# Performance work log

Measured on AMD Instinct MI355X. Metric: run time of the kernel, lower is better.

## Reference

```python
import jax, jax.numpy as jnp
import numpy as np

B, L = 2, 1024
D_MODEL, N_LAYER = 768, 2
D_INNER, D_STATE, D_CONV, DT_RANK = 1536, 16, 4, 48
D_INT, VOCAB = 1536, 32000
EPS = 1e-5


def layernorm(x, w, b):
    m = x.mean(-1, keepdims=True)
    v = ((x - m) ** 2).mean(-1, keepdims=True)
    return (x - m) * jax.lax.rsqrt(v + EPS) * w + b


def silu(x):
    return x * jax.nn.sigmoid(x)


def depthwise_causal_conv(x, w, b):
    # x: (B,L,D); w: (D,K) torch depthwise weight squeezed; b: (D,)
    k = w.shape[-1]
    kern = w.T[:, None, :]  # (K,1,D) for 'WIO' with feature_group_count=D
    y = jax.lax.conv_general_dilated(
        x, kern, window_strides=(1,), padding=[(k - 1, 0)],
        dimension_numbers=('NWC', 'WIO', 'NWC'),
        feature_group_count=x.shape[-1])
    return y + b


def selective_scan(u, delta, A, Bm, Cm, Dp):
    # u, delta: (B,L,Dn); A: (Dn,N); Bm, Cm: (B,L,N); Dp: (Dn,)
    dA = jnp.exp(delta[..., None] * A)                         # (B,L,Dn,N)
    dBu = delta[..., None] * Bm[:, :, None, :] * u[..., None]  # (B,L,Dn,N)

    def step(h, inp):
        dA_t, dBu_t, C_t = inp
        h = dA_t * h + dBu_t
        return h, jnp.einsum('bdn,bn->bd', h, C_t)

    h0 = jnp.zeros((u.shape[0], A.shape[0], A.shape[1]), u.dtype)
    _, ys = jax.lax.scan(step, h0, (jnp.swapaxes(dA, 0, 1), jnp.swapaxes(dBu, 0, 1), jnp.swapaxes(Cm, 0, 1)))
    return jnp.swapaxes(ys, 0, 1) + u * Dp


def mamba_mixer(x, p):
    xz = x @ p['in_proj'].T                     # (B,L,2*Dn)
    xin, z = jnp.split(xz, 2, axis=-1)
    xc = silu(depthwise_causal_conv(xin, p['conv_w'], p['conv_b']))
    x_dbl = xc @ p['x_proj'].T                  # (B,L,dt_rank+2N)
    dt, Bm, Cm = jnp.split(x_dbl, [DT_RANK, DT_RANK + D_STATE], axis=-1)
    delta = jax.nn.softplus(dt @ p['dt_w'].T + p['dt_b'])
    A = -jnp.exp(p['A_log'])
    y = selective_scan(xc, delta, A, Bm, Cm, p['D'])
    y = y * silu(z)
    return y @ p['out_proj'].T


def block(h, res, p):
    # mamba_ssm Block (non-fused path) with GatedMLP
    res = h + res if res is not None else h
    x = layernorm(res, p['norm_w'], p['norm_b'])
    x = mamba_mixer(x, p)
    res = x + res
    x = layernorm(res, p['norm2_w'], p['norm2_b'])
    y, gate = jnp.split(x @ p['fc1'].T, 2, axis=-1)
    x = (y * silu(gate)) @ p['fc2'].T
    return x, res


def _forward(input_ids, embed, norm_w, norm_b, in_proj, conv_w, conv_b, x_proj,
             dt_w, dt_b, A_log, D, out_proj, norm2_w, norm2_b, fc1, fc2,
             normf_w, normf_b):
    h = embed[input_ids]
    res = None
    for i in range(N_LAYER):
        p = dict(norm_w=norm_w[i], norm_b=norm_b[i], in_proj=in_proj[i],
                 conv_w=conv_w[i], conv_b=conv_b[i], x_proj=x_proj[i],
                 dt_w=dt_w[i], dt_b=dt_b[i], A_log=A_log[i], D=D[i],
                 out_proj=out_proj[i], norm2_w=norm2_w[i], norm2_b=norm2_b[i],
                 fc1=fc1[i], fc2=fc2[i])
        h_f, r_f = block(h, res, p)
        h_f = layernorm(h_f, normf_w, normf_b)
        res_flip = res[:, ::-1] if res is not None else None
        h_b, r_b = block(h[:, ::-1], res_flip, p)
        h_b = layernorm(h_b, normf_w, normf_b)
        h = h_f + h_b[:, ::-1]
        res = r_f + r_b[:, ::-1]
    # dropout is identity at inference
    res = h + res
    h = layernorm(res, normf_w, normf_b)
    return h.mean(axis=1)  # (B, d_model)


def setup_inputs() -> dict:
    key = jax.random.key(0)
    ks = iter(jax.random.split(key, 32))

    def rn(shape, scale=0.02):
        return jax.random.normal(next(ks), shape, jnp.float32) * scale

    inp = {}
    inp['input_ids'] = jax.random.randint(next(ks), (B, L), 0, VOCAB)
    inp['embed'] = rn((VOCAB, D_MODEL))
    inp['norm_w'] = jnp.ones((N_LAYER, D_MODEL), jnp.float32)
    inp['norm_b'] = jnp.zeros((N_LAYER, D_MODEL), jnp.float32)
    inp['in_proj'] = rn((N_LAYER, 2 * D_INNER, D_MODEL))
    inp['conv_w'] = rn((N_LAYER, D_INNER, D_CONV), 0.2)
    inp['conv_b'] = jnp.zeros((N_LAYER, D_INNER), jnp.float32)
    inp['x_proj'] = rn((N_LAYER, DT_RANK + 2 * D_STATE, D_INNER))
    inp['dt_w'] = rn((N_LAYER, D_INNER, DT_RANK), 0.1)
    # inverse-softplus of ~0.01 so delta starts small (matches mamba dt init spirit)
    inp['dt_b'] = jnp.full((N_LAYER, D_INNER), float(np.log(np.expm1(0.01))), jnp.float32)
    # S4D-real init: A = -(1..d_state)
    inp['A_log'] = jnp.broadcast_to(jnp.log(jnp.arange(1, D_STATE + 1, dtype=jnp.float32)), (N_LAYER, D_INNER, D_STATE)).copy()
    inp['D'] = jnp.ones((N_LAYER, D_INNER), jnp.float32)
    inp['out_proj'] = rn((N_LAYER, D_MODEL, D_INNER))
    inp['norm2_w'] = jnp.ones((N_LAYER, D_MODEL), jnp.float32)
    inp['norm2_b'] = jnp.zeros((N_LAYER, D_MODEL), jnp.float32)
    inp['fc1'] = rn((N_LAYER, 2 * D_INT, D_MODEL))
    inp['fc2'] = rn((N_LAYER, D_MODEL, D_INT))
    inp['normf_w'] = jnp.ones((D_MODEL,), jnp.float32)
    inp['normf_b'] = jnp.zeros((D_MODEL,), jnp.float32)
    return inp


def reference(input_ids, embed, norm_w, norm_b, in_proj, conv_w, conv_b, x_proj,
              dt_w, dt_b, A_log, D, out_proj, norm2_w, norm2_b, fc1, fc2,
              normf_w, normf_b):
    return _forward(input_ids, embed, norm_w, norm_b, in_proj, conv_w, conv_b,
                    x_proj, dt_w, dt_b, A_log, D, out_proj, norm2_w, norm2_b,
                    fc1, fc2, normf_w, normf_b)
```

## Files before the change

kernel.cpp:

```cpp
#include <hip/hip_runtime.h>
#include <cstddef>

#define BB 2
#define LL 1024
#define DM 768
#define DI 1536
#define NST 16
#define DTR 48
#define DINT 1536
#define NLAYER 2
#define ML (BB*LL)
#define NCH 32
#define CLEN (LL/NCH)

typedef __attribute__((ext_vector_type(8))) short s16x8;
typedef __attribute__((ext_vector_type(4))) float f32x4;

static __device__ __forceinline__ float sigm(float x){ return 1.f/(1.f+__expf(-x)); }
static __device__ __forceinline__ float silu_(float x){ return x*sigm(x); }
static __device__ __forceinline__ float softplus_(float x){ return fmaxf(x,0.f)+log1pf(__expf(-fabsf(x))); }
static __device__ __forceinline__ unsigned short f2b(float x){
  unsigned int u = __float_as_uint(x);
  unsigned int r = (u + 0x7fffu + ((u>>16)&1u)) >> 16;
  return (unsigned short)r;
}
static __device__ __forceinline__ float b2f(unsigned short v){
  return __uint_as_float(((unsigned int)v) << 16);
}

__global__ void k_embed(const int* __restrict__ ids, const float* __restrict__ emb,
                        float* __restrict__ out){
  int idx = blockIdx.x*256 + threadIdx.x;
  if (idx >= ML*DM) return;
  int c = idx % DM; int bl = idx / DM;
  out[idx] = emb[(size_t)ids[bl]*DM + c];
}

__global__ void k_add(const float* __restrict__ a, const float* __restrict__ b,
                      float* __restrict__ c, int n){
  int idx = blockIdx.x*256 + threadIdx.x;
  if (idx >= n) return;
  c[idx] = a[idx] + b[idx];
}

__global__ void k_f2b(const float* __restrict__ in, unsigned short* __restrict__ out, int n){
  int idx = blockIdx.x*256 + threadIdx.x;
  if (idx >= n) return;
  out[idx] = f2b(in[idx]);
}

__global__ void k_weff(const float* __restrict__ dw, const float* __restrict__ xp,
                       unsigned short* __restrict__ wbig){
  int idx = blockIdx.x*256 + threadIdx.x;
  int j = idx % DI, i = idx / DI;
  float s = 0.f;
  #pragma unroll
  for (int k = 0; k < DTR; k++) s += dw[i*DTR + k] * xp[(size_t)k*DI + j];
  wbig[idx] = f2b(s);
}

__global__ void k_wtail(const float* __restrict__ xp, unsigned short* __restrict__ wbig){
  int idx = blockIdx.x*256 + threadIdx.x;
  if (idx >= 128*DI) return;
  int j = idx % DI, r = idx / DI;
  unsigned short v = (r < 32) ? f2b(xp[(size_t)(DTR + r)*DI + j]) : (unsigned short)0;
  wbig[(size_t)(DI + r)*DI + j] = v;
}

__global__ __launch_bounds__(256) void k_ln(const float* __restrict__ x,
    const float* __restrict__ add, const float* __restrict__ w, const float* __restrict__ bi,
    float* __restrict__ sumout, float* __restrict__ fout, unsigned short* __restrict__ bout,
    int acc, int rows){
  int wv = threadIdx.x >> 6, lane = threadIdx.x & 63;
  int row = blockIdx.x*4 + wv;
  if (row >= rows) return;
  const float* xr = x + (size_t)row*DM;
  float v[12]; float s = 0.f, sq = 0.f;
  #pragma unroll
  for (int i = 0; i < 12; i++){
    int c = lane + 64*i;
    float t = xr[c];
    if (add) t += add[(size_t)row*DM + c];
    if (sumout) sumout[(size_t)row*DM + c] = t;
    v[i] = t; s += t; sq += t*t;
  }
  #pragma unroll
  for (int o = 32; o; o >>= 1){ s += __shfl_xor(s, o, 64); sq += __shfl_xor(sq, o, 64); }
  float mean = s*(1.f/DM);
  float var  = sq*(1.f/DM) - mean*mean;
  float rstd = rsqrtf(var + 1e-5f);
  #pragma unroll
  for (int i = 0; i < 12; i++){
    int c = lane + 64*i;
    float o = (v[i]-mean)*rstd*w[c] + bi[c];
    if (fout){
      float oo = o;
      if (acc) oo += fout[(size_t)row*DM + c];
      fout[(size_t)row*DM + c] = oo;
    }
    if (bout) bout[(size_t)row*DM + c] = f2b(o);
  }
}

static __device__ __forceinline__ void mgemm_core(
    const unsigned short* __restrict__ A, const unsigned short* __restrict__ W, int K,
    unsigned short* As, unsigned short* Bs, f32x4 (&acc)[4][4]){
  int t = threadIdx.x;
  int m0 = blockIdx.y*128, n0 = blockIdx.x*128;
  int lane = t & 63, w = t >> 6;
  int wm = w & 1, wn = w >> 1;
  for (int k0 = 0; k0 < K; k0 += 32){
    #pragma unroll
    for (int si = 0; si < 2; si++){
      int s = t + si*256;
      int row = ((s>>6)<<4) + (s & 15);
      int ko  = ((s>>4) & 3) << 3;
      *(uint4*)&As[s*8] = *(const uint4*)&A[(size_t)(m0+row)*K + k0 + ko];
      *(uint4*)&Bs[s*8] = *(const uint4*)&W[(size_t)(n0+row)*K + k0 + ko];
    }
    __syncthreads();
    s16x8 af[4], bf[4];
    #pragma unroll
    for (int i = 0; i < 4; i++) af[i] = *(const s16x8*)&As[((wm*4+i)*64 + lane)*8];
    #pragma unroll
    for (int j = 0; j < 4; j++) bf[j] = *(const s16x8*)&Bs[((wn*4+j)*64 + lane)*8];
    #pragma unroll
    for (int i = 0; i < 4; i++)
      #pragma unroll
      for (int j = 0; j < 4; j++)
        acc[i][j] = __builtin_amdgcn_mfma_f32_16x16x32_bf16(af[i], bf[j], acc[i][j], 0, 0, 0);
    __syncthreads();
  }
}

__global__ __launch_bounds__(256) void k_mgemm0(const unsigned short* __restrict__ A,
    const unsigned short* __restrict__ W, const float* __restrict__ addsrc,
    float* __restrict__ Cf, int N, int K){
  __shared__ __align__(16) unsigned short As[4096], Bs[4096];
  f32x4 acc[4][4] = {};
  mgemm_core(A, W, K, As, Bs, acc);
  int t = threadIdx.x, lane = t & 63, w = t >> 6;
  int wm = w & 1, wn = w >> 1;
  int m0 = blockIdx.y*128, n0 = blockIdx.x*128;
  int cl = lane & 15, qd = lane >> 4;
  #pragma unroll
  for (int i = 0; i < 4; i++){
    int mbase = m0 + (wm*4+i)*16 + qd*4;
    #pragma unroll
    for (int j = 0; j < 4; j++){
      int n = n0 + (wn*4+j)*16 + cl;
      #pragma unroll
      for (int r = 0; r < 4; r++){
        int m = mbase + r;
        float v = acc[i][j][r];
        if (addsrc) v += addsrc[(size_t)(m & (ML-1))*N + n];
        Cf[(size_t)m*N + n] = v;
      }
    }
  }
}

__global__ __launch_bounds__(256) void k_mgemm1(const unsigned short* __restrict__ A,
    const unsigned short* __restrict__ W, const float* __restrict__ dtb,
    unsigned short* __restrict__ dlb, float* __restrict__ bcout, int K){
  __shared__ __align__(16) unsigned short As[4096], Bs[4096];
  f32x4 acc[4][4] = {};
  mgemm_core(A, W, K, As, Bs, acc);
  int t = threadIdx.x, lane = t & 63, w = t >> 6;
  int wm = w & 1, wn = w >> 1;
  int m0 = blockIdx.y*128, n0 = blockIdx.x*128;
  int cl = lane & 15, qd = lane >> 4;
  #pragma unroll
  for (int i = 0; i < 4; i++){
    int mbase = m0 + (wm*4+i)*16 + qd*4;
    #pragma unroll
    for (int j = 0; j < 4; j++){
      int n = n0 + (wn*4+j)*16 + cl;
      #pragma unroll
      for (int r = 0; r < 4; r++){
        int m = mbase + r;
        float v = acc[i][j][r];
        if (n < DI) dlb[(size_t)m*DI + n] = f2b(softplus_(v + dtb[n]));
        else if (n < DI + 32) bcout[(size_t)m*32 + (n - DI)] = v;
      }
    }
  }
}

__global__ __launch_bounds__(256) void k_mgemm2(const unsigned short* __restrict__ A,
    const unsigned short* __restrict__ W, unsigned short* __restrict__ Cb, int N, int K){
  __shared__ __align__(16) unsigned short As[4096], Bs[4096];
  f32x4 acc[4][4] = {};
  mgemm_core(A, W, K, As, Bs, acc);
  int t = threadIdx.x, lane = t & 63, w = t >> 6;
  int wm = w & 1, wn = w >> 1;
  int m0 = blockIdx.y*128, n0 = blockIdx.x*128;
  int cl = lane & 15, qd = lane >> 4;
  #pragma unroll
  for (int i = 0; i < 4; i++){
    int mbase = m0 + (wm*4+i)*16 + qd*4;
    #pragma unroll
    for (int j = 0; j < 4; j++){
      int n = n0 + (wn*4+j)*16 + cl;
      #pragma unroll
      for (int r = 0; r < 4; r++){
        int m = mbase + r;
        Cb[(size_t)m*N + n] = f2b(acc[i][j][r]);
      }
    }
  }
}

__global__ void k_conv(const float* __restrict__ xz, const float* __restrict__ w,
                       const float* __restrict__ bi, unsigned short* __restrict__ xcb){
  int idx = blockIdx.x*256 + threadIdx.x;
  if (idx >= 2*ML*DI) return;
  int d = idx % DI; int r = idx / DI;
  int bl = r % ML; int dir = r / ML;
  int t = bl % LL; int b = bl / LL;
  float acc = bi[d];
  #pragma unroll
  for (int k = 0; k < 4; k++){
    int tp = dir ? (t + 3 - k) : (t - 3 + k);
    if (tp >= 0 && tp < LL)
      acc += w[d*4 + k] * xz[((size_t)(b*LL + tp))*(2*DI) + d];
  }
  xcb[idx] = f2b(silu_(acc));
}

__global__ __launch_bounds__(256) void k_scan1(
    const unsigned short* __restrict__ dlb, const unsigned short* __restrict__ xcb,
    const float* __restrict__ bc, const float* __restrict__ A_log,
    float* __restrict__ sA, float* __restrict__ sH){
  __shared__ float Bsh[CLEN*16];
  int blk = blockIdx.x;
  int dgrp = blk % (DI/256); int rest = blk / (DI/256);
  int ch = rest % NCH; rest /= NCH;
  int b = rest & 1; int dir = rest >> 1;
  int d = dgrp*256 + threadIdx.x;
  int t0 = dir ? (LL-1 - ch*CLEN) : ch*CLEN;
  long step = dir ? -1 : 1;
  long row0 = (long)dir*ML + b*LL + t0;
  #pragma unroll
  for (int rep = 0; rep < CLEN*16/256; rep++){
    int e = threadIdx.x + rep*256;
    int s = e >> 4, n = e & 15;
    Bsh[e] = bc[(size_t)(row0 + s*step)*32 + n];
  }
  __syncthreads();
  float ea[16];
  #pragma unroll
  for (int n = 0; n < 16; n++) ea[n] = -__expf(A_log[d*16 + n]) * 1.44269504f;
  float h[16], P[16];
  #pragma unroll
  for (int n = 0; n < 16; n++){ h[n] = 0.f; P[n] = 1.f; }
  long row = row0;
  for (int s = 0; s < CLEN; s++){
    float de = b2f(dlb[(size_t)row*DI + d]);
    float u  = b2f(xcb[(size_t)row*DI + d]);
    float duu = de*u;
    float Ba[16];
    const f32x4* Bv = (const f32x4*)&Bsh[s*16];
    *(f32x4*)&Ba[0] = Bv[0]; *(f32x4*)&Ba[4] = Bv[1];
    *(f32x4*)&Ba[8] = Bv[2]; *(f32x4*)&Ba[12] = Bv[3];
    #pragma unroll
    for (int n = 0; n < 16; n++){
      float dA = exp2f(de*ea[n]);
      h[n] = dA*h[n] + duu*Ba[n];
      P[n] *= dA;
    }
    row += step;
  }
  size_t sbase = ((((size_t)dir*BB + b)*NCH + ch)*DI + d)*16;
  #pragma unroll
  for (int n = 0; n < 16; n++){ sA[sbase+n] = P[n]; sH[sbase+n] = h[n]; }
}

__global__ __launch_bounds__(256) void k_prefix(
    const float* __restrict__ sA, const float* __restrict__ sH, float* __restrict__ h0){
  int gid = blockIdx.x*256 + threadIdx.x;
  int dn = gid % (DI*16);
  int db_ = gid / (DI*16);
  float h = 0.f;
  size_t base = (size_t)db_*NCH*DI*16 + dn;
  for (int ch = 0; ch < NCH; ch++){
    size_t idx = base + (size_t)ch*DI*16;
    h0[idx] = h;
    h = sH[idx] + sA[idx]*h;
  }
}

__global__ __launch_bounds__(256) void k_scan2(
    const unsigned short* __restrict__ dlb, const unsigned short* __restrict__ xcb,
    const float* __restrict__ bc, const float* __restrict__ xz,
    const float* __restrict__ A_log, const float* __restrict__ Dp,
    const float* __restrict__ h0, unsigned short* __restrict__ y){
  __shared__ float BCs[CLEN*32];
  int blk = blockIdx.x;
  int dgrp = blk % (DI/256); int rest = blk / (DI/256);
  int ch = rest % NCH; rest /= NCH;
  int b = rest & 1; int dir = rest >> 1;
  int d = dgrp*256 + threadIdx.x;
  int t0 = dir ? (LL-1 - ch*CLEN) : ch*CLEN;
  long step = dir ? -1 : 1;
  long row0 = (long)dir*ML + b*LL + t0;
  #pragma unroll
  for (int rep = 0; rep < CLEN*32/256; rep++){
    int e = threadIdx.x + rep*256;
    int s = e >> 5, n = e & 31;
    BCs[e] = bc[(size_t)(row0 + s*step)*32 + n];
  }
  __syncthreads();
  float ea[16];
  #pragma unroll
  for (int n = 0; n < 16; n++) ea[n] = -__expf(A_log[d*16 + n]) * 1.44269504f;
  float dD = Dp[d];
  float h[16];
  size_t hbase = ((((size_t)dir*BB + b)*NCH + ch)*DI + d)*16;
  #pragma unroll
  for (int n = 0; n < 16; n++) h[n] = h0[hbase + n];
  long row = row0;
  long zoff = (long)dir*ML;
  for (int s = 0; s < CLEN; s++){
    float de = b2f(dlb[(size_t)row*DI + d]);
    float u  = b2f(xcb[(size_t)row*DI + d]);
    float z  = xz[(size_t)(row - zoff)*(2*DI) + DI + d];
    float duu = de*u;
    float Ba[16], Ca[16];
    const f32x4* Bv = (const f32x4*)&BCs[s*32];
    *(f32x4*)&Ba[0] = Bv[0]; *(f32x4*)&Ba[4] = Bv[1];
    *(f32x4*)&Ba[8] = Bv[2]; *(f32x4*)&Ba[12] = Bv[3];
    *(f32x4*)&Ca[0] = Bv[4]; *(f32x4*)&Ca[4] = Bv[5];
    *(f32x4*)&Ca[8] = Bv[6]; *(f32x4*)&Ca[12] = Bv[7];
    float p0 = 0.f, p1 = 0.f, p2 = 0.f, p3 = 0.f;
    #pragma unroll
    for (int n = 0; n < 16; n += 4){
      float dA0 = exp2f(de*ea[n]),   dA1 = exp2f(de*ea[n+1]);
      float dA2 = exp2f(de*ea[n+2]), dA3 = exp2f(de*ea[n+3]);
      h[n]   = dA0*h[n]   + duu*Ba[n];
      h[n+1] = dA1*h[n+1] + duu*Ba[n+1];
      h[n+2] = dA2*h[n+2] + duu*Ba[n+2];
      h[n+3] = dA3*h[n+3] + duu*Ba[n+3];
      p0 = fmaf(h[n],   Ca[n],   p0);
      p1 = fmaf(h[n+1], Ca[n+1], p1);
      p2 = fmaf(h[n+2], Ca[n+2], p2);
      p3 = fmaf(h[n+3], Ca[n+3], p3);
    }
    float p = (p0+p1) + (p2+p3);
    y[(size_t)row*DI + d] = f2b((p + u*dD) * silu_(z));
    row += step;
  }
}

__global__ void k_gate(const unsigned short* __restrict__ fc1o, unsigned short* __restrict__ g){
  int idx = blockIdx.x*256 + threadIdx.x;
  if (idx >= 2*ML*DINT) return;
  int i = idx % DINT; int bl = idx / DINT;
  float aa = b2f(fc1o[(size_t)bl*2*DINT + i]);
  float gt = b2f(fc1o[(size_t)bl*2*DINT + DINT + i]);
  g[idx] = f2b(aa * silu_(gt));
}

__global__ void k_mean(const float* __restrict__ x, float* __restrict__ out){
  int d = blockIdx.x*256 + threadIdx.x;
  int b = blockIdx.y;
  if (d >= DM) return;
  float s = 0.f;
  for (int t = 0; t < LL; t++) s += x[((size_t)(b*LL + t))*DM + d];
  out[b*DM + d] = s*(1.f/LL);
}

extern "C" void kernel_launch(void* const* d_in, const int* in_sizes, int n_in,
                              void* d_out, int out_size, void* d_ws, size_t ws_size,
                              hipStream_t stream){
  const int*   ids     = (const int*)d_in[0];
  const float* embed   = (const float*)d_in[1];
  const float* norm_w  = (const float*)d_in[2];
  const float* norm_b  = (const float*)d_in[3];
  const float* in_proj = (const float*)d_in[4];
  const float* conv_w  = (const float*)d_in[5];
  const float* conv_b  = (const float*)d_in[6];
  const float* x_proj  = (const float*)d_in[7];
  const float* dt_w    = (const float*)d_in[8];
  const float* dt_b    = (const float*)d_in[9];
  const float* A_log   = (const float*)d_in[10];
  const float* Dp      = (const float*)d_in[11];
  const float* out_pj  = (const float*)d_in[12];
  const float* norm2_w = (const float*)d_in[13];
  const float* norm2_b = (const float*)d_in[14];
  const float* fc1     = (const float*)d_in[15];
  const float* fc2     = (const float*)d_in[16];
  const float* normf_w = (const float*)d_in[17];
  const float* normf_b = (const float*)d_in[18];
  float* out = (float*)d_out;

  const size_t BLD   = (size_t)ML*DM;
  const size_t BLDI  = (size_t)ML*DI;
  const size_t BL2DI = (size_t)ML*2*DI;
  const size_t SUMN  = (size_t)2*BB*NCH*DI*16;

  float* f = (float*)d_ws; size_t off = 0;
  float* h     = f+off; off += BLD;
  float* res   = f+off; off += BLD;
  float* rc    = f+off; off += BLD;
  float* resd  = f+off; off += 2*BLD;
  float* xz    = f+off; off += BL2DI;
  float* bc    = f+off; off += (size_t)2*ML*32;
  float* sA    = f+off; off += SUMN;
  float* sH    = f+off; off += SUMN;
  float* h0    = f+off; off += SUMN;
  float*          mlpo = xz;
  unsigned short* gb   = (unsigned short*)sA;
  unsigned short* u16 = (unsigned short*)(f + off); size_t uo = 0;
  unsigned short* xlnb = u16+uo; uo += BLD;
  unsigned short* x2b  = u16+uo; uo += 2*BLD;
  unsigned short* xcb  = u16+uo; uo += 2*BLDI;
  unsigned short* dlb  = u16+uo; uo += 2*BLDI;
  unsigned short* wib  = u16+uo; uo += (size_t)2*DI*DM;
  unsigned short* wob  = u16+uo; uo += (size_t)DM*DI;
  unsigned short* wbig = u16+uo; uo += (size_t)1664*DI;
  unsigned short* yb   = xcb;
  unsigned short* fc1o = xcb;
  unsigned short* wf1b = wib;
  unsigned short* wf2b = wob;
  (void)ws_size; (void)in_sizes; (void)n_in; (void)out_size;

  dim3 blk(256);
  auto cdiv = [](int a, int b){ return (a + b - 1)/b; };
  const int scan_blocks = 2*2*NCH*(DI/256);

  k_embed<<<cdiv(ML*DM,256), blk, 0, stream>>>(ids, embed, h);

  for (int l = 0; l < NLAYER; l++){
    const float* nw  = norm_w  + l*DM;
    const float* nb  = norm_b  + l*DM;
    const float* ip  = in_proj + (size_t)l*2*DI*DM;
    const float* cw  = conv_w  + (size_t)l*DI*4;
    const float* cb  = conv_b  + (size_t)l*DI;
    const float* xp  = x_proj  + (size_t)l*(DTR+2*NST)*DI;
    const float* dw  = dt_w    + (size_t)l*DI*DTR;
    const float* db  = dt_b    + (size_t)l*DI;
    const float* al  = A_log   + (size_t)l*DI*NST;
    const float* dpl = Dp      + (size_t)l*DI;
    const float* op  = out_pj  + (size_t)l*DM*DI;
    const float* n2w = norm2_w + l*DM;
    const float* n2b = norm2_b + l*DM;
    const float* f1  = fc1 + (size_t)l*2*DINT*DM;
    const float* f2  = fc2 + (size_t)l*DM*DINT;

    k_f2b<<<cdiv(2*DI*DM,256), blk, 0, stream>>>(ip, wib, 2*DI*DM);
    k_f2b<<<cdiv(DM*DI,256), blk, 0, stream>>>(op, wob, DM*DI);
    k_weff<<<cdiv(DI*DI,256), blk, 0, stream>>>(dw, xp, wbig);
    k_wtail<<<cdiv(128*DI,256), blk, 0, stream>>>(xp, wbig);

    k_ln<<<ML/4, blk, 0, stream>>>(h, (l==0)?nullptr:res, nw, nb, rc, nullptr, xlnb, 0, ML);
    k_mgemm0<<<dim3(2*DI/128, ML/128), blk, 0, stream>>>(xlnb, wib, nullptr, xz, 2*DI, DM);
    k_conv<<<cdiv(2*ML*DI,256), blk, 0, stream>>>(xz, cw, cb, xcb);
    k_mgemm1<<<dim3(1664/128, 2*ML/128), blk, 0, stream>>>(xcb, wbig, db, dlb, bc, DI);
    k_scan1<<<scan_blocks, blk, 0, stream>>>(dlb, xcb, bc, al, sA, sH);
    k_prefix<<<(2*BB*DI*16)/256, blk, 0, stream>>>(sA, sH, h0);
    k_scan2<<<scan_blocks, blk, 0, stream>>>(dlb, xcb, bc, xz, al, dpl, h0, yb);
    k_f2b<<<cdiv(2*DINT*DM,256), blk, 0, stream>>>(f1, wf1b, 2*DINT*DM);
    k_mgemm0<<<dim3(DM/128, 2*ML/128), blk, 0, stream>>>(yb, wob, rc, resd, DM, DI);
    k_f2b<<<cdiv(DM*DINT,256), blk, 0, stream>>>(f2, wf2b, DM*DINT);
    k_ln<<<2*ML/4, blk, 0, stream>>>(resd, nullptr, n2w, n2b, nullptr, nullptr, x2b, 0, 2*ML);
    k_mgemm2<<<dim3(2*DINT/128, 2*ML/128), blk, 0, stream>>>(x2b, wf1b, fc1o, 2*DINT, DM);
    k_gate<<<cdiv(2*ML*DINT,256), blk, 0, stream>>>(fc1o, gb);
    k_mgemm0<<<dim3(DM/128, 2*ML/128), blk, 0, stream>>>(gb, wf2b, nullptr, mlpo, DM, DINT);
    k_ln<<<ML/4, blk, 0, stream>>>(mlpo, nullptr, normf_w, normf_b, nullptr, h, nullptr, 0, ML);
    k_ln<<<ML/4, blk, 0, stream>>>(mlpo + BLD, nullptr, normf_w, normf_b, nullptr, h, nullptr, 1, ML);
    k_add<<<cdiv(ML*DM,256), blk, 0, stream>>>(resd, resd + BLD, res, ML*DM);
  }

  k_ln<<<ML/4, blk, 0, stream>>>(h, res, normf_w, normf_b, nullptr, rc, nullptr, 0, ML);
  k_mean<<<dim3(3, BB), blk, 0, stream>>>(rc, out);
}
```

Before: 1.286 ms.

## Batch weight conversion, shrink GEMM N-tile, store xz in bf16, fuse final layernorms

All bf16 weight conversions for both layers now run up front in one segmented kernel, plus a merged dt/x_proj weight builder. The GEMM tile shrinks from 128x128 to 128x64 to launch more blocks on the small-N projections. The in_proj output xz is stored as bf16 instead of fp32, which halves its traffic in conv and scan2 at some precision cost. The two per-branch layernorms and the residual add are fused into one kernel, and the prefix kernel writes h0 in place over sA to save a buffer.

```diff
diff --git a/kernel.cpp b/kernel.cpp
--- a/kernel.cpp
+++ b/kernel.cpp
@@ -36,41 +36,39 @@
   out[idx] = emb[(size_t)ids[bl]*DM + c];
 }
 
-__global__ void k_add(const float* __restrict__ a, const float* __restrict__ b,
-                      float* __restrict__ c, int n){
+struct Seg8 { const float* src[8]; unsigned short* dst[8]; int cum[9]; };
+__global__ void k_f2bseg(Seg8 p){
   int idx = blockIdx.x*256 + threadIdx.x;
-  if (idx >= n) return;
-  c[idx] = a[idx] + b[idx];
-}
-
-__global__ void k_f2b(const float* __restrict__ in, unsigned short* __restrict__ out, int n){
+  if (idx >= p.cum[8]) return;
+  int s = 0;
+  #pragma unroll
+  for (int i = 1; i < 8; i++) s += (idx >= p.cum[i]);
+  int local = idx - p.cum[s];
+  p.dst[s][local] = f2b(p.src[s][local]);
+}
+
+__global__ void k_wbig(const float* __restrict__ dw, const float* __restrict__ xp,
+                       unsigned short* __restrict__ wb){
   int idx = blockIdx.x*256 + threadIdx.x;
-  if (idx >= n) return;
-  out[idx] = f2b(in[idx]);
-}
-
-__global__ void k_weff(const float* __restrict__ dw, const float* __restrict__ xp,
-                       unsigned short* __restrict__ wbig){
-  int idx = blockIdx.x*256 + threadIdx.x;
+  if (idx >= 1664*DI) return;
   int j = idx % DI, i = idx / DI;
-  float s = 0.f;
-  #pragma unroll
-  for (int k = 0; k < DTR; k++) s += dw[i*DTR + k] * xp[(size_t)k*DI + j];
-  wbig[idx] = f2b(s);
-}
-
-__global__ void k_wtail(const float* __restrict__ xp, unsigned short* __restrict__ wbig){
-  int idx = blockIdx.x*256 + threadIdx.x;
-  if (idx >= 128*DI) return;
-  int j = idx % DI, r = idx / DI;
-  unsigned short v = (r < 32) ? f2b(xp[(size_t)(DTR + r)*DI + j]) : (unsigned short)0;
-  wbig[(size_t)(DI + r)*DI + j] = v;
+  unsigned short v;
+  if (i < DI){
+    float s = 0.f;
+    #pragma unroll
+    for (int k = 0; k < DTR; k++) s += dw[i*DTR + k] * xp[(size_t)k*DI + j];
+    v = f2b(s);
+  } else {
+    int r = i - DI;
+    v = (r < 32) ? f2b(xp[(size_t)(DTR + r)*DI + j]) : (unsigned short)0;
+  }
+  wb[idx] = v;
 }
 
 __global__ __launch_bounds__(256) void k_ln(const float* __restrict__ x,
     const float* __restrict__ add, const float* __restrict__ w, const float* __restrict__ bi,
     float* __restrict__ sumout, float* __restrict__ fout, unsigned short* __restrict__ bout,
-    int acc, int rows){
+    int rows){
   int wv = threadIdx.x >> 6, lane = threadIdx.x & 63;
   int row = blockIdx.x*4 + wv;
   if (row >= rows) return;
@@ -93,20 +91,48 @@
   for (int i = 0; i < 12; i++){
     int c = lane + 64*i;
     float o = (v[i]-mean)*rstd*w[c] + bi[c];
-    if (fout){
-      float oo = o;
-      if (acc) oo += fout[(size_t)row*DM + c];
-      fout[(size_t)row*DM + c] = oo;
-    }
+    if (fout) fout[(size_t)row*DM + c] = o;
     if (bout) bout[(size_t)row*DM + c] = f2b(o);
+  }
+}
+
+__global__ __launch_bounds__(256) void k_lnfin(const float* __restrict__ mlpo,
+    const float* __restrict__ resd, const float* __restrict__ w, const float* __restrict__ bi,
+    float* __restrict__ h, float* __restrict__ res){
+  int wv = threadIdx.x >> 6, lane = threadIdx.x & 63;
+  int row = blockIdx.x*4 + wv;
+  if (row >= ML) return;
+  const float* x0 = mlpo + (size_t)row*DM;
+  const float* x1 = mlpo + (size_t)(ML + row)*DM;
+  float v0[12], v1[12]; float s0=0,q0=0,s1=0,q1=0;
+  #pragma unroll
+  for (int i = 0; i < 12; i++){
+    int c = lane + 64*i;
+    float a = x0[c], b = x1[c];
+    v0[i]=a; v1[i]=b; s0+=a; q0+=a*a; s1+=b; q1+=b*b;
+  }
+  #pragma unroll
+  for (int o = 32; o; o >>= 1){
+    s0 += __shfl_xor(s0, o, 64); q0 += __shfl_xor(q0, o, 64);
+    s1 += __shfl_xor(s1, o, 64); q1 += __shfl_xor(q1, o, 64);
+  }
+  float m0 = s0*(1.f/DM), m1 = s1*(1.f/DM);
+  float r0 = rsqrtf(q0*(1.f/DM) - m0*m0 + 1e-5f);
+  float r1 = rsqrtf(q1*(1.f/DM) - m1*m1 + 1e-5f);
+  #pragma unroll
+  for (int i = 0; i < 12; i++){
+    int c = lane + 64*i;
+    float o = ((v0[i]-m0)*r0 + (v1[i]-m1)*r1)*w[c] + 2.f*bi[c];
+    h[(size_t)row*DM + c] = o;
+    res[(size_t)row*DM + c] = resd[(size_t)row*DM + c] + resd[(size_t)(ML+row)*DM + c];
   }
 }
 
 static __device__ __forceinline__ void mgemm_core(
     const unsigned short* __restrict__ A, const unsigned short* __restrict__ W, int K,
-    unsigned short* As, unsigned short* Bs, f32x4 (&acc)[4][4]){
+    unsigned short* As, unsigned short* Bs, f32x4 (&acc)[4][2]){
   int t = threadIdx.x;
-  int m0 = blockIdx.y*128, n0 = blockIdx.x*128;
+  int m0 = blockIdx.y*128, n0 = blockIdx.x*64;
   int lane = t & 63, w = t >> 6;
   int wm = w & 1, wn = w >> 1;
   for (int k0 = 0; k0 < K; k0 += 32){
@@ -116,39 +142,44 @@
       int row = ((s>>6)<<4) + (s & 15);
       int ko  = ((s>>4) & 3) << 3;
       *(uint4*)&As[s*8] = *(const uint4*)&A[(size_t)(m0+row)*K + k0 + ko];
+    }
+    {
+      int s = t;
+      int row = ((s>>6)<<4) + (s & 15);
+      int ko  = ((s>>4) & 3) << 3;
       *(uint4*)&Bs[s*8] = *(const uint4*)&W[(size_t)(n0+row)*K + k0 + ko];
     }
     __syncthreads();
-    s16x8 af[4], bf[4];
+    s16x8 af[4], bf[2];
     #pragma unroll
     for (int i = 0; i < 4; i++) af[i] = *(const s16x8*)&As[((wm*4+i)*64 + lane)*8];
     #pragma unroll
-    for (int j = 0; j < 4; j++) bf[j] = *(const s16x8*)&Bs[((wn*4+j)*64 + lane)*8];
+    for (int j = 0; j < 2; j++) bf[j] = *(const s16x8*)&Bs[((wn*2+j)*64 + lane)*8];
     #pragma unroll
     for (int i = 0; i < 4; i++)
       #pragma unroll
-      for (int j = 0; j < 4; j++)
+      for (int j = 0; j < 2; j++)
         acc[i][j] = __builtin_amdgcn_mfma_f32_16x16x32_bf16(af[i], bf[j], acc[i][j], 0, 0, 0);
     __syncthreads();
   }
 }
 
-__global__ __launch_bounds__(256) void k_mgemm0(const unsigned short* __restrict__ A,
+__global__ __launch_bounds__(256) void k_mg0(const unsigned short* __restrict__ A,
     const unsigned short* __restrict__ W, const float* __restrict__ addsrc,
     float* __restrict__ Cf, int N, int K){
-  __shared__ __align__(16) unsigned short As[4096], Bs[4096];
-  f32x4 acc[4][4] = {};
+  __shared__ __align__(16) unsigned short As[4096], Bs[2048];
+  f32x4 acc[4][2] = {};
   mgemm_core(A, W, K, As, Bs, acc);
   int t = threadIdx.x, lane = t & 63, w = t >> 6;
   int wm = w & 1, wn = w >> 1;
-  int m0 = blockIdx.y*128, n0 = blockIdx.x*128;
+  int m0 = blockIdx.y*128, n0 = blockIdx.x*64;
   int cl = lane & 15, qd = lane >> 4;
   #pragma unroll
   for (int i = 0; i < 4; i++){
     int mbase = m0 + (wm*4+i)*16 + qd*4;
     #pragma unroll
-    for (int j = 0; j < 4; j++){
-      int n = n0 + (wn*4+j)*16 + cl;
+    for (int j = 0; j < 2; j++){
+      int n = n0 + (wn*2+j)*16 + cl;
       #pragma unroll
       for (int r = 0; r < 4; r++){
         int m = mbase + r;
@@ -160,22 +191,22 @@
   }
 }
 
-__global__ __launch_bounds__(256) void k_mgemm1(const unsigned short* __restrict__ A,
+__global__ __launch_bounds__(256) void k_mg1(const unsigned short* __restrict__ A,
     const unsigned short* __restrict__ W, const float* __restrict__ dtb,
     unsigned short* __restrict__ dlb, float* __restrict__ bcout, int K){
-  __shared__ __align__(16) unsigned short As[4096], Bs[4096];
-  f32x4 acc[4][4] = {};
+  __shared__ __align__(16) unsigned short As[4096], Bs[2048];
+  f32x4 acc[4][2] = {};
   mgemm_core(A, W, K, As, Bs, acc);
   int t = threadIdx.x, lane = t & 63, w = t >> 6;
   int wm = w & 1, wn = w >> 1;
-  int m0 = blockIdx.y*128, n0 = blockIdx.x*128;
+  int m0 = blockIdx.y*128, n0 = blockIdx.x*64;
   int cl = lane & 15, qd = lane >> 4;
   #pragma unroll
   for (int i = 0; i < 4; i++){
     int mbase = m0 + (wm*4+i)*16 + qd*4;
     #pragma unroll
-    for (int j = 0; j < 4; j++){
-      int n = n0 + (wn*4+j)*16 + cl;
+    for (int j = 0; j < 2; j++){
+      int n = n0 + (wn*2+j)*16 + cl;
       #pragma unroll
       for (int r = 0; r < 4; r++){
         int m = mbase + r;
@@ -187,21 +218,21 @@
   }
 }
 
-__global__ __launch_bounds__(256) void k_mgemm2(const unsigned short* __restrict__ A,
+__global__ __launch_bounds__(256) void k_mg2(const unsigned short* __restrict__ A,
     const unsigned short* __restrict__ W, unsigned short* __restrict__ Cb, int N, int K){
-  __shared__ __align__(16) unsigned short As[4096], Bs[4096];
-  f32x4 acc[4][4] = {};
+  __shared__ __align__(16) unsigned short As[4096], Bs[2048];
+  f32x4 acc[4][2] = {};
   mgemm_core(A, W, K, As, Bs, acc);
   int t = threadIdx.x, lane = t & 63, w = t >> 6;
   int wm = w & 1, wn = w >> 1;
-  int m0 = blockIdx.y*128, n0 = blockIdx.x*128;
+  int m0 = blockIdx.y*128, n0 = blockIdx.x*64;
   int cl = lane & 15, qd = lane >> 4;
   #pragma unroll
   for (int i = 0; i < 4; i++){
     int mbase = m0 + (wm*4+i)*16 + qd*4;
     #pragma unroll
-    for (int j = 0; j < 4; j++){
-      int n = n0 + (wn*4+j)*16 + cl;
+    for (int j = 0; j < 2; j++){
+      int n = n0 + (wn*2+j)*16 + cl;
       #pragma unroll
       for (int r = 0; r < 4; r++){
         int m = mbase + r;
@@ -211,7 +242,7 @@
   }
 }
 
-__global__ void k_conv(const float* __restrict__ xz, const float* __restrict__ w,
+__global__ void k_conv(const unsigned short* __restrict__ xzb, const float* __restrict__ w,
                        const float* __restrict__ bi, unsigned short* __restrict__ xcb){
   int idx = blockIdx.x*256 + threadIdx.x;
   if (idx >= 2*ML*DI) return;
@@ -223,7 +254,7 @@
   for (int k = 0; k < 4; k++){
     int tp = dir ? (t + 3 - k) : (t - 3 + k);
     if (tp >= 0 && tp < LL)
-      acc += w[d*4 + k] * xz[((size_t)(b*LL + tp))*(2*DI) + d];
+      acc += w[d*4 + k] * b2f(xzb[((size_t)(b*LL + tp))*(2*DI) + d]);
   }
   xcb[idx] = f2b(silu_(acc));
 }
@@ -277,7 +308,7 @@
 }
 
 __global__ __launch_bounds__(256) void k_prefix(
-    const float* __restrict__ sA, const float* __restrict__ sH, float* __restrict__ h0){
+    float* __restrict__ sA, const float* __restrict__ sH){
   int gid = blockIdx.x*256 + threadIdx.x;
   int dn = gid % (DI*16);
   int db_ = gid / (DI*16);
@@ -285,14 +316,15 @@
   size_t base = (size_t)db_*NCH*DI*16 + dn;
   for (int ch = 0; ch < NCH; ch++){
     size_t idx = base + (size_t)ch*DI*16;
-    h0[idx] = h;
-    h = sH[idx] + sA[idx]*h;
+    float a = sA[idx], hh = sH[idx];
+    sA[idx] = h;
+    h = hh + a*h;
   }
 }
 
 __global__ __launch_bounds__(256) void k_scan2(
     const unsigned short* __restrict__ dlb, const unsigned short* __restrict__ xcb,
-    const float* __restrict__ bc, const float* __restrict__ xz,
+    const float* __restrict__ bc, const unsigned short* __restrict__ xzb,
     const float* __restrict__ A_log, const float* __restrict__ Dp,
     const float* __restrict__ h0, unsigned short* __restrict__ y){
   __shared__ float BCs[CLEN*32];
@@ -324,7 +356,7 @@
   for (int s = 0; s < CLEN; s++){
     float de = b2f(dlb[(size_t)row*DI + d]);
     float u  = b2f(xcb[(size_t)row*DI + d]);
-    float z  = xz[(size_t)(row - zoff)*(2*DI) + DI + d];
+    float z  = b2f(xzb[(size_t)(row - zoff)*(2*DI) + DI + d]);
     float duu = de*u;
     float Ba[16], Ca[16];
     const f32x4* Bv = (const f32x4*)&BCs[s*32];
@@ -396,7 +428,6 @@
 
   const size_t BLD   = (size_t)ML*DM;
   const size_t BLDI  = (size_t)ML*DI;
-  const size_t BL2DI = (size_t)ML*2*DI;
   const size_t SUMN  = (size_t)2*BB*NCH*DI*16;
 
   float* f = (float*)d_ws; size_t off = 0;
@@ -404,74 +435,78 @@
   float* res   = f+off; off += BLD;
   float* rc    = f+off; off += BLD;
   float* resd  = f+off; off += 2*BLD;
-  float* xz    = f+off; off += BL2DI;
   float* bc    = f+off; off += (size_t)2*ML*32;
   float* sA    = f+off; off += SUMN;
   float* sH    = f+off; off += SUMN;
-  float* h0    = f+off; off += SUMN;
-  float*          mlpo = xz;
-  unsigned short* gb   = (unsigned short*)sA;
+  unsigned short* gb = (unsigned short*)sH;
   unsigned short* u16 = (unsigned short*)(f + off); size_t uo = 0;
   unsigned short* xlnb = u16+uo; uo += BLD;
   unsigned short* x2b  = u16+uo; uo += 2*BLD;
+  unsigned short* xzb  = u16+uo; uo += 2*BLDI;
   unsigned short* xcb  = u16+uo; uo += 2*BLDI;
   unsigned short* dlb  = u16+uo; uo += 2*BLDI;
-  unsigned short* wib  = u16+uo; uo += (size_t)2*DI*DM;
-  unsigned short* wob  = u16+uo; uo += (size_t)DM*DI;
-  unsigned short* wbig = u16+uo; uo += (size_t)1664*DI;
+  unsigned short* wts  = u16+uo;
+  const size_t W_IP = (size_t)2*DI*DM, W_OP = (size_t)DM*DI, W_F1 = (size_t)2*DINT*DM,
+               W_F2 = (size_t)DM*DINT, W_BG = (size_t)1664*DI;
+  const size_t WLAY = W_IP + W_OP + W_F1 + W_F2 + W_BG;
   unsigned short* yb   = xcb;
   unsigned short* fc1o = xcb;
-  unsigned short* wf1b = wib;
-  unsigned short* wf2b = wob;
+  float*          mlpo = (float*)xcb;
   (void)ws_size; (void)in_sizes; (void)n_in; (void)out_size;
 
   dim3 blk(256);
   auto cdiv = [](int a, int b){ return (a + b - 1)/b; };
   const int scan_blocks = 2*2*NCH*(DI/256);
 
+  Seg8 sg; int cum = 0;
+  for (int l = 0; l < 2; l++){
+    unsigned short* wl = wts + (size_t)l*WLAY;
+    sg.src[l*4+0] = in_proj + (size_t)l*W_IP; sg.dst[l*4+0] = wl;
+    sg.src[l*4+1] = out_pj  + (size_t)l*W_OP; sg.dst[l*4+1] = wl + W_IP;
+    sg.src[l*4+2] = fc1     + (size_t)l*W_F1; sg.dst[l*4+2] = wl + W_IP + W_OP;
+    sg.src[l*4+3] = fc2     + (size_t)l*W_F2; sg.dst[l*4+3] = wl + W_IP + W_OP + W_F1;
+  }
+  { int sz[8] = {(int)W_IP,(int)W_OP,(int)W_F1,(int)W_F2,(int)W_IP,(int)W_OP,(int)W_F1,(int)W_F2};
+    sg.cum[0]=0; for (int i = 0; i < 8; i++){ cum += sz[i]; sg.cum[i+1] = cum; } }
+  k_f2bseg<<<cdiv(cum,256), blk, 0, stream>>>(sg);
+  for (int l = 0; l < 2; l++)
+    k_wbig<<<cdiv(1664*DI,256), blk, 0, stream>>>(dt_w + (size_t)l*DI*DTR,
+        x_proj + (size_t)l*(DTR+2*NST)*DI, wts + (size_t)l*WLAY + W_IP + W_OP + W_F1 + W_F2);
+
   k_embed<<<cdiv(ML*DM,256), blk, 0, stream>>>(ids, embed, h);
 
   for (int l = 0; l < NLAYER; l++){
+    unsigned short* wl   = wts + (size_t)l*WLAY;
+    unsigned short* wib  = wl;
+    unsigned short* wob  = wl + W_IP;
+    unsigned short* wf1b = wl + W_IP + W_OP;
+    unsigned short* wf2b = wl + W_IP + W_OP + W_F1;
+    unsigned short* wbig = wl + W_IP + W_OP + W_F1 + W_F2;
     const float* nw  = norm_w  + l*DM;
     const float* nb  = norm_b  + l*DM;
-    const float* ip  = in_proj + (size_t)l*2*DI*DM;
     const float* cw  = conv_w  + (size_t)l*DI*4;
     const float* cb  = conv_b  + (size_t)l*DI;
-    const float* xp  = x_proj  + (size_t)l*(DTR+2*NST)*DI;
-    const float* dw  = dt_w    + (size_t)l*DI*DTR;
     const float* db  = dt_b    + (size_t)l*DI;
     const float* al  = A_log   + (size_t)l*DI*NST;
     const float* dpl = Dp      + (size_t)l*DI;
-    const float* op  = out_pj  + (size_t)l*DM*DI;
     const float* n2w = norm2_w + l*DM;
     const float* n2b = norm2_b + l*DM;
-    const float* f1  = fc1 + (size_t)l*2*DINT*DM;
-    const float* f2  = fc2 + (size_t)l*DM*DINT;
-
-    k_f2b<<<cdiv(2*DI*DM,256), blk, 0, stream>>>(ip, wib, 2*DI*DM);
-    k_f2b<<<cdiv(DM*DI,256), blk, 0, stream>>>(op, wob, DM*DI);
-    k_weff<<<cdiv(DI*DI,256), blk, 0, stream>>>(dw, xp, wbig);
-    k_wtail<<<cdiv(128*DI,256), blk, 0, stream>>>(xp, wbig);
-
-    k_ln<<<ML/4, blk, 0, stream>>>(h, (l==0)?nullptr:res, nw, nb, rc, nullptr, xlnb, 0, ML);
-    k_mgemm0<<<dim3(2*DI/128, ML/128), blk, 0, stream>>>(xlnb, wib, nullptr, xz, 2*DI, DM);
-    k_conv<<<cdiv(2*ML*DI,256), blk, 0, stream>>>(xz, cw, cb, xcb);
-    k_mgemm1<<<dim3(1664/128, 2*ML/128), blk, 0, stream>>>(xcb, wbig, db, dlb, bc, DI);
+
+    k_ln<<<ML/4, blk, 0, stream>>>(h, (l==0)?nullptr:res, nw, nb, rc, nullptr, xlnb, ML);
+    k_mg2<<<dim3(2*DI/64, ML/128), blk, 0, stream>>>(xlnb, wib, xzb, 2*DI, DM);
+    k_conv<<<cdiv(2*ML*DI,256), blk, 0, stream>>>(xzb, cw, cb, xcb);
+    k_mg1<<<dim3(1664/64, 2*ML/128), blk, 0, stream>>>(xcb, wbig, db, dlb, bc, DI);
     k_scan1<<<scan_blocks, blk, 0, stream>>>(dlb, xcb, bc, al, sA, sH);
-    k_prefix<<<(2*BB*DI*16)/256, blk, 0, stream>>>(sA, sH, h0);
-    k_scan2<<<scan_blocks, blk, 0, stream>>>(dlb, xcb, bc, xz, al, dpl, h0, yb);
-    k_f2b<<<cdiv(2*DINT*DM,256), blk, 0, stream>>>(f1, wf1b, 2*DINT*DM);
-    k_mgemm0<<<dim3(DM/128, 2*ML/128), blk, 0, stream>>>(yb, wob, rc, resd, DM, DI);
-    k_f2b<<<cdiv(DM*DINT,256), blk, 0, stream>>>(f2, wf2b, DM*DINT);
-    k_ln<<<2*ML/4, blk, 0, stream>>>(resd, nullptr, n2w, n2b, nullptr, nullptr, x2b, 0, 2*ML);
-    k_mgemm2<<<dim3(2*DINT/128, 2*ML/128), blk, 0, stream>>>(x2b, wf1b, fc1o, 2*DINT, DM);
+    k_prefix<<<(2*BB*DI*16)/256, blk, 0, stream>>>(sA, sH);
+    k_scan2<<<scan_blocks, blk, 0, stream>>>(dlb, xcb, bc, xzb, al, dpl, sA, yb);
+    k_mg0<<<dim3(DM/64, 2*ML/128), blk, 0, stream>>>(yb, wob, rc, resd, DM, DI);
+    k_ln<<<2*ML/4, blk, 0, stream>>>(resd, nullptr, n2w, n2b, nullptr, nullptr, x2b, 2*ML);
+    k_mg2<<<dim3(2*DINT/64, 2*ML/128), blk, 0, stream>>>(x2b, wf1b, fc1o, 2*DINT, DM);
     k_gate<<<cdiv(2*ML*DINT,256), blk, 0, stream>>>(fc1o, gb);
-    k_mgemm0<<<dim3(DM/128, 2*ML/128), blk, 0, stream>>>(gb, wf2b, nullptr, mlpo, DM, DINT);
-    k_ln<<<ML/4, blk, 0, stream>>>(mlpo, nullptr, normf_w, normf_b, nullptr, h, nullptr, 0, ML);
-    k_ln<<<ML/4, blk, 0, stream>>>(mlpo + BLD, nullptr, normf_w, normf_b, nullptr, h, nullptr, 1, ML);
-    k_add<<<cdiv(ML*DM,256), blk, 0, stream>>>(resd, resd + BLD, res, ML*DM);
-  }
-
-  k_ln<<<ML/4, blk, 0, stream>>>(h, res, normf_w, normf_b, nullptr, rc, nullptr, 0, ML);
+    k_mg0<<<dim3(DM/64, 2*ML/128), blk, 0, stream>>>(gb, wf2b, nullptr, mlpo, DM, DINT);
+    k_lnfin<<<ML/4, blk, 0, stream>>>(mlpo, resd, normf_w, normf_b, h, res);
+  }
+
+  k_ln<<<ML/4, blk, 0, stream>>>(h, res, normf_w, normf_b, nullptr, rc, nullptr, ML);
   k_mean<<<dim3(3, BB), blk, 0, stream>>>(rc, out);
 }
```

After: 1.231 ms. 1.04x faster.
